# Kernel tuning notes

Hardware: AMD Instinct MI355X
Metric: run time of the kernel (lower is better)

Reference implementation:

```python
import jax, jax.numpy as jnp
import numpy as np

KH, KW = 2, 3          # kernel_size of the masked (shifted) conv
CW = KW // 2           # width padding for order 'A'
B, C, H, W = 8, 32, 256, 256
HID = 64


def _wn(v, g):
    # weight normalization: w = g * v / ||v||, norm over (in, kh, kw) per out channel
    norm = jnp.sqrt(jnp.sum(v * v, axis=(1, 2, 3), keepdims=True))
    return v * (g[:, None, None, None] / norm)


def _conv(x, w, b):
    y = jax.lax.conv_general_dilated(
        x, w, window_strides=(1, 1), padding='VALID',
        dimension_numbers=('NCHW', 'OIHW', 'NCHW'))
    return y + b[None, :, None, None]


def setup_inputs() -> dict:
    key = jax.random.key(0)
    ks = jax.random.split(key, 4)
    x = jax.random.normal(ks[0], (B, C, H, W), dtype=jnp.float32)
    v1 = jax.random.normal(ks[1], (HID, C, KH, KW), dtype=jnp.float32) * 0.05
    g1 = jnp.ones((HID,), dtype=jnp.float32)
    b1 = jnp.zeros((HID,), dtype=jnp.float32)
    v2 = jax.random.normal(ks[2], (2 * C, HID, 1, 1), dtype=jnp.float32) * 0.05
    g2 = jnp.ones((2 * C,), dtype=jnp.float32)
    b2 = jnp.zeros((2 * C,), dtype=jnp.float32)
    return {"x": x, "v1": v1, "g1": g1, "b1": b1, "v2": v2, "g2": g2, "b2": b2}


def reference(x, v1, g1, b1, v2, g2, b2):
    # ShiftedConv2d, order 'A': pad KH rows on top, CW cols each side, drop last
    # row, then VALID conv -> output at row h only sees input rows h-KH..h-1.
    xs = jnp.pad(x, ((0, 0), (0, 0), (KH, 0), (CW, CW)))[:, :, :-1, :]
    h = _conv(xs, _wn(v1, g1), b1)                 # [B, HID, H, W]
    h = jax.nn.elu(h)
    ms = _conv(h, _wn(v2, g2), b2)                 # [B, 2C, H, W]
    mu, log_scale = jnp.split(ms, 2, axis=1)
    scale = jax.nn.sigmoid(log_scale + 2.0)
    out = x * scale + mu                           # affine flow
    logdet = jnp.sum(jnp.log(scale).reshape(x.shape[0], -1), axis=1)  # [B]
    return out, logdet
```

## Files before the change

kernel.cpp:

```cpp
#include <hip/hip_runtime.h>
#include <hip/hip_bf16.h>
#include <math.h>

#define B_   8
#define C_   32
#define H_   256
#define W_   256
#define HW_  (H_*W_)
#define NPIX (B_*C_*H_*W_)

#define PW    260
#define ROWDW (PW*16)
#define ROWB  (ROWDW*4)

typedef __attribute__((ext_vector_type(8))) short short8;
typedef __attribute__((ext_vector_type(4))) float f32x4;
typedef __attribute__((ext_vector_type(2))) float f32x2;

static __device__ __forceinline__ short f2bf(float f) {
    union { __hip_bfloat16 h; short s; } u; u.h = __float2bfloat16(f); return u.s;
}
static __device__ __forceinline__ int cvtpk(float lo, float hi) {
    int r;
    asm("v_cvt_pk_bf16_f32 %0, %1, %2" : "=v"(r) : "v"(lo), "v"(hi));
    return r;
}

__global__ __launch_bounds__(64) void prep_kernel(
    const float* __restrict__ v1, const float* __restrict__ g1,
    const float* __restrict__ v2, const float* __restrict__ g2,
    short* __restrict__ w1b, short* __restrict__ w2b)
{
    const int t   = threadIdx.x;
    const int bid = blockIdx.x;
    if (bid < 64) {
        const int o = bid;
        float a0 = v1[o*192 + t];
        float a1 = v1[o*192 + t + 64];
        float a2 = v1[o*192 + t + 128];
        float s  = a0*a0 + a1*a1 + a2*a2;
        #pragma unroll
        for (int m = 32; m >= 1; m >>= 1) s += __shfl_xor(s, m, 64);
        const float inv = g1[o] / sqrtf(s);
        const int e0 = t, e1 = t + 64, e2 = t + 128;
        w1b[o*192 + (e0%6)*32 + e0/6] = f2bf(a0*inv);
        w1b[o*192 + (e1%6)*32 + e1/6] = f2bf(a1*inv);
        w1b[o*192 + (e2%6)*32 + e2/6] = f2bf(a2*inv);
    } else {
        const int j = bid - 64;
        float a = v2[j*64 + t];
        float s = a*a;
        #pragma unroll
        for (int m = 32; m >= 1; m >>= 1) s += __shfl_xor(s, m, 64);
        const float inv = g2[j] / sqrtf(s);
        const int mt = t >> 4, r = t & 15;
        const int slot = (mt >> 1)*32 + ((r >> 2) << 3) + ((mt & 1) << 2) + (r & 3);
        w2b[j*64 + slot] = f2bf(a*inv);
    }
}

__global__ __launch_bounds__(256) void flow_kernel(
    const float* __restrict__ x,
    const short* __restrict__ w1b, const short* __restrict__ w2b,
    const float* __restrict__ b1,  const float* __restrict__ b2,
    float* __restrict__ out, float* __restrict__ ldpart)
{
    __shared__ int ldsI[2*ROWDW];

    const int bi0 = blockIdx.x;
    const int bi  = (bi0 & 7) * 256 + (bi0 >> 3);
    const int b   = bi >> 8;
    const int h   = bi & 255;

    const int tid  = threadIdx.x;
    const int l    = tid & 63;
    const int wv   = tid >> 6;
    const int lrow = l & 15;
    const int q    = l >> 4;

    const float* xb = x + (size_t)b * (C_*HW_);
    float* ob       = out + (size_t)b * (C_*HW_);

    {
        const int r   = tid >> 7;
        const int hr  = h - 2 + r;
        const int u   = tid & 127;
        const int w0  = u << 1;
        const int p0  = w0 + 1, p1 = w0 + 2;
        const int sw0 = (p0 >> 2) & 3, sw1 = (p1 >> 2) & 3;
        if (hr >= 0) {
            const float* pr = xb + (size_t)hr * W_ + w0;
            #pragma unroll
            for (int g = 0; g < 4; ++g) {
                f32x2 a[8];
                #pragma unroll
                for (int j = 0; j < 8; ++j)
                    a[j] = *(const f32x2*)(pr + (size_t)(8*g + j) * HW_);
                int4 d0, d1;
                d0.x = cvtpk(a[0][0], a[1][0]); d0.y = cvtpk(a[2][0], a[3][0]);
                d0.z = cvtpk(a[4][0], a[5][0]); d0.w = cvtpk(a[6][0], a[7][0]);
                d1.x = cvtpk(a[0][1], a[1][1]); d1.y = cvtpk(a[2][1], a[3][1]);
                d1.z = cvtpk(a[4][1], a[5][1]); d1.w = cvtpk(a[6][1], a[7][1]);
                *(int4*)&ldsI[r*ROWDW + p0*16 + ((g ^ sw0) << 2)] = d0;
                *(int4*)&ldsI[r*ROWDW + p1*16 + ((g ^ sw1) << 2)] = d1;
            }
        } else {
            const int4 z4 = {0,0,0,0};
            #pragma unroll
            for (int g = 0; g < 4; ++g) {
                *(int4*)&ldsI[r*ROWDW + p0*16 + ((g ^ sw0) << 2)] = z4;
                *(int4*)&ldsI[r*ROWDW + p1*16 + ((g ^ sw1) << 2)] = z4;
            }
        }
        if (tid < 16) {
            const int rz = tid >> 3;
            const int pz = ((tid >> 2) & 1) ? 257 : 0;
            *(int4*)&ldsI[rz*ROWDW + pz*16 + ((tid & 3) << 2)] = (int4){0,0,0,0};
        }
    }
    __syncthreads();

    const int cb0 = h*W_ + wv*64 + lrow;
    float xv[8][4];
    #pragma unroll
    for (int jj = 0; jj < 8; ++jj) {
        const int j = (jj >> 2)*16 + 4*q + (jj & 3);
        const float* pxj = xb + (size_t)j * HW_ + cb0;
        #pragma unroll
        for (int nt = 0; nt < 4; ++nt)
            xv[jj][nt] = pxj[nt*16];
    }

    f32x4 acc1[4][4];
    #pragma unroll
    for (int mt = 0; mt < 4; ++mt) {
        const f32x4 bv = *(const f32x4*)(b1 + mt*16 + 4*q);
        #pragma unroll
        for (int nt = 0; nt < 4; ++nt) acc1[mt][nt] = bv;
    }

    #pragma unroll
    for (int tap = 0; tap < 6; ++tap) {
        const int rb = (tap < 3) ? 0 : ROWB;
        const int dw = (tap % 3) - 1;
        short8 wf[4];
        #pragma unroll
        for (int mt = 0; mt < 4; ++mt)
            wf[mt] = *(const short8*)(w1b + (mt*16 + lrow)*192 + tap*32 + q*8);
        #pragma unroll
        for (int nt = 0; nt < 4; ++nt) {
            const int p = wv*64 + nt*16 + lrow + dw + 1;
            const int byteoff = rb + p*64 + ((q ^ ((p >> 2) & 3)) << 4);
            const short8 xf = *(const short8*)((const char*)ldsI + byteoff);
            #pragma unroll
            for (int mt = 0; mt < 4; ++mt)
                acc1[mt][nt] = __builtin_amdgcn_mfma_f32_16x16x32_bf16(
                                   wf[mt], xf, acc1[mt][nt], 0, 0, 0);
        }
    }

    int4 up0[4], up1[4];
    #pragma unroll
    for (int nt = 0; nt < 4; ++nt) {
        float e[16];
        #pragma unroll
        for (int mt = 0; mt < 4; ++mt)
            #pragma unroll
            for (int rg = 0; rg < 4; ++rg) {
                const float v = acc1[mt][nt][rg];
                e[mt*4 + rg] = v > 0.f ? v : (__expf(v) - 1.f);
            }
        up0[nt].x = cvtpk(e[0],  e[1]);  up0[nt].y = cvtpk(e[2],  e[3]);
        up0[nt].z = cvtpk(e[4],  e[5]);  up0[nt].w = cvtpk(e[6],  e[7]);
        up1[nt].x = cvtpk(e[8],  e[9]);  up1[nt].y = cvtpk(e[10], e[11]);
        up1[nt].z = cvtpk(e[12], e[13]); up1[nt].w = cvtpk(e[14], e[15]);
    }

    short8 a2f[2][4];
    #pragma unroll
    for (int kt = 0; kt < 2; ++kt)
        #pragma unroll
        for (int mt2 = 0; mt2 < 4; ++mt2)
            a2f[kt][mt2] = *(const short8*)(w2b + (mt2*16 + lrow)*64 + kt*32 + q*8);

    f32x4 b2m[2], b2s[2];
    #pragma unroll
    for (int mt2 = 0; mt2 < 2; ++mt2) {
        b2m[mt2] = *(const f32x4*)(b2 + mt2*16 + 4*q);
        b2s[mt2] = *(const f32x4*)(b2 + 32 + mt2*16 + 4*q);
    }

    float ldsum = 0.f;
    #pragma unroll
    for (int nt = 0; nt < 4; ++nt) {
        union { int4 i; short8 s; } u0, u1;
        u0.i = up0[nt];
        u1.i = up1[nt];

        f32x4 acc2[4];
        #pragma unroll
        for (int mt2 = 0; mt2 < 4; ++mt2) {
            f32x4 t0 = __builtin_amdgcn_mfma_f32_16x16x32_bf16(
                           a2f[0][mt2], u0.s, (f32x4){0.f,0.f,0.f,0.f}, 0, 0, 0);
            acc2[mt2] = __builtin_amdgcn_mfma_f32_16x16x32_bf16(
                           a2f[1][mt2], u1.s, t0, 0, 0, 0);
        }

        float pr8 = 1.f;
        #pragma unroll
        for (int mt2 = 0; mt2 < 2; ++mt2)
            #pragma unroll
            for (int rg = 0; rg < 4; ++rg) {
                const int jj = mt2*4 + rg;
                const int j  = mt2*16 + 4*q + rg;
                const float mu = acc2[mt2][rg]     + b2m[mt2][rg];
                const float z  = acc2[mt2 + 2][rg] + b2s[mt2][rg] + 2.f;
                const float sc = 1.f / (1.f + __expf(-z));
                pr8 *= sc;
                ob[(size_t)j * HW_ + cb0 + nt*16] = xv[jj][nt] * sc + mu;
            }
        ldsum += __logf(pr8);
    }

    #pragma unroll
    for (int m = 32; m >= 1; m >>= 1) ldsum += __shfl_xor(ldsum, m, 64);
    if (l == 0) ldpart[(size_t)bi * 4 + wv] = ldsum;
}

__global__ __launch_bounds__(256) void reduce_kernel(
    const float* __restrict__ ldpart, float* __restrict__ logdet)
{
    __shared__ float r4[4];
    const int b = blockIdx.x;
    const int t = threadIdx.x;
    const f32x4 v = *(const f32x4*)(ldpart + (size_t)b*1024 + t*4);
    float s = v[0] + v[1] + v[2] + v[3];
    #pragma unroll
    for (int m = 32; m >= 1; m >>= 1) s += __shfl_xor(s, m, 64);
    if ((t & 63) == 0) r4[t >> 6] = s;
    __syncthreads();
    if (t == 0) logdet[b] = r4[0] + r4[1] + r4[2] + r4[3];
}

extern "C" void kernel_launch(void* const* d_in, const int* in_sizes, int n_in,
                              void* d_out, int out_size, void* d_ws, size_t ws_size,
                              hipStream_t stream)
{
    const float* x  = (const float*)d_in[0];
    const float* v1 = (const float*)d_in[1];
    const float* g1 = (const float*)d_in[2];
    const float* b1 = (const float*)d_in[3];
    const float* v2 = (const float*)d_in[4];
    const float* g2 = (const float*)d_in[5];
    const float* b2 = (const float*)d_in[6];

    float* out    = (float*)d_out;
    float* logdet = out + NPIX;

    short* w1b    = (short*)d_ws;
    short* w2b    = w1b + 12288;
    float* ldpart = (float*)((char*)d_ws + 32768);

    prep_kernel<<<128, 64, 0, stream>>>(v1, g1, v2, g2, w1b, w2b);
    flow_kernel<<<B_ * H_, 256, 0, stream>>>(x, w1b, w2b, b1, b2, out, ldpart);
    reduce_kernel<<<B_, 256, 0, stream>>>(ldpart, logdet);
}
```

Measured before the change: 63.04 us.

## Process two output rows per block reusing staged input row in LDS

Each block now computes two consecutive output rows and keeps the shared middle input row resident in a two-slot LDS ring buffer. For the second row it stages only one new row, so each block loads three input rows for two outputs instead of four. The grid is halved and the logdet partial layout and reduce kernel are resized to match. The price is an extra pair of barriers that serialize staging and compute within a block, plus fewer blocks to hide latency.

```diff
diff --git a/kernel.cpp b/kernel.cpp
--- a/kernel.cpp
+++ b/kernel.cpp
@@ -67,10 +67,10 @@
 {
     __shared__ int ldsI[2*ROWDW];
 
-    const int bi0 = blockIdx.x;
-    const int bi  = (bi0 & 7) * 256 + (bi0 >> 3);
-    const int b   = bi >> 8;
-    const int h   = bi & 255;
+    const int bi0  = blockIdx.x;
+    const int b    = bi0 & 7;
+    const int rest = bi0 >> 3;
+    const int h0   = rest << 1;
 
     const int tid  = threadIdx.x;
     const int l    = tid & 63;
@@ -81,17 +81,17 @@
     const float* xb = x + (size_t)b * (C_*HW_);
     float* ob       = out + (size_t)b * (C_*HW_);
 
-    {
-        const int r   = tid >> 7;
-        const int hr  = h - 2 + r;
+    auto stage_row = [&](int hr, int slotdw) {
         const int u   = tid & 127;
         const int w0  = u << 1;
         const int p0  = w0 + 1, p1 = w0 + 2;
         const int sw0 = (p0 >> 2) & 3, sw1 = (p1 >> 2) & 3;
+        const int gb  = (tid >> 7) << 1;
         if (hr >= 0) {
             const float* pr = xb + (size_t)hr * W_ + w0;
             #pragma unroll
-            for (int g = 0; g < 4; ++g) {
+            for (int gg = 0; gg < 2; ++gg) {
+                const int g = gb + gg;
                 f32x2 a[8];
                 #pragma unroll
                 for (int j = 0; j < 8; ++j)
@@ -101,130 +101,146 @@
                 d0.z = cvtpk(a[4][0], a[5][0]); d0.w = cvtpk(a[6][0], a[7][0]);
                 d1.x = cvtpk(a[0][1], a[1][1]); d1.y = cvtpk(a[2][1], a[3][1]);
                 d1.z = cvtpk(a[4][1], a[5][1]); d1.w = cvtpk(a[6][1], a[7][1]);
-                *(int4*)&ldsI[r*ROWDW + p0*16 + ((g ^ sw0) << 2)] = d0;
-                *(int4*)&ldsI[r*ROWDW + p1*16 + ((g ^ sw1) << 2)] = d1;
+                *(int4*)&ldsI[slotdw + p0*16 + ((g ^ sw0) << 2)] = d0;
+                *(int4*)&ldsI[slotdw + p1*16 + ((g ^ sw1) << 2)] = d1;
             }
         } else {
             const int4 z4 = {0,0,0,0};
             #pragma unroll
-            for (int g = 0; g < 4; ++g) {
-                *(int4*)&ldsI[r*ROWDW + p0*16 + ((g ^ sw0) << 2)] = z4;
-                *(int4*)&ldsI[r*ROWDW + p1*16 + ((g ^ sw1) << 2)] = z4;
-            }
-        }
-        if (tid < 16) {
-            const int rz = tid >> 3;
-            const int pz = ((tid >> 2) & 1) ? 257 : 0;
-            *(int4*)&ldsI[rz*ROWDW + pz*16 + ((tid & 3) << 2)] = (int4){0,0,0,0};
-        }
+            for (int gg = 0; gg < 2; ++gg) {
+                const int g = gb + gg;
+                *(int4*)&ldsI[slotdw + p0*16 + ((g ^ sw0) << 2)] = z4;
+                *(int4*)&ldsI[slotdw + p1*16 + ((g ^ sw1) << 2)] = z4;
+            }
+        }
+    };
+
+    auto compute_row = [&](int h, int rbA, int rbB) -> float {
+        const int cb0 = h*W_ + wv*64 + lrow;
+        float xv[8][4];
+        #pragma unroll
+        for (int jj = 0; jj < 8; ++jj) {
+            const int j = (jj >> 2)*16 + 4*q + (jj & 3);
+            const float* pxj = xb + (size_t)j * HW_ + cb0;
+            #pragma unroll
+            for (int nt = 0; nt < 4; ++nt)
+                xv[jj][nt] = pxj[nt*16];
+        }
+
+        f32x4 acc1[4][4];
+        #pragma unroll
+        for (int mt = 0; mt < 4; ++mt) {
+            const f32x4 bv = *(const f32x4*)(b1 + mt*16 + 4*q);
+            #pragma unroll
+            for (int nt = 0; nt < 4; ++nt) acc1[mt][nt] = bv;
+        }
+
+        #pragma unroll
+        for (int tap = 0; tap < 6; ++tap) {
+            const int rb = (tap < 3) ? rbA : rbB;
+            const int dw = (tap % 3) - 1;
+            short8 wf[4];
+            #pragma unroll
+            for (int mt = 0; mt < 4; ++mt)
+                wf[mt] = *(const short8*)(w1b + (mt*16 + lrow)*192 + tap*32 + q*8);
+            #pragma unroll
+            for (int nt = 0; nt < 4; ++nt) {
+                const int p = wv*64 + nt*16 + lrow + dw + 1;
+                const int byteoff = rb + p*64 + ((q ^ ((p >> 2) & 3)) << 4);
+                const short8 xf = *(const short8*)((const char*)ldsI + byteoff);
+                #pragma unroll
+                for (int mt = 0; mt < 4; ++mt)
+                    acc1[mt][nt] = __builtin_amdgcn_mfma_f32_16x16x32_bf16(
+                                       wf[mt], xf, acc1[mt][nt], 0, 0, 0);
+            }
+        }
+
+        int4 up0[4], up1[4];
+        #pragma unroll
+        for (int nt = 0; nt < 4; ++nt) {
+            float e[16];
+            #pragma unroll
+            for (int mt = 0; mt < 4; ++mt)
+                #pragma unroll
+                for (int rg = 0; rg < 4; ++rg) {
+                    const float v = acc1[mt][nt][rg];
+                    e[mt*4 + rg] = v > 0.f ? v : (__expf(v) - 1.f);
+                }
+            up0[nt].x = cvtpk(e[0],  e[1]);  up0[nt].y = cvtpk(e[2],  e[3]);
+            up0[nt].z = cvtpk(e[4],  e[5]);  up0[nt].w = cvtpk(e[6],  e[7]);
+            up1[nt].x = cvtpk(e[8],  e[9]);  up1[nt].y = cvtpk(e[10], e[11]);
+            up1[nt].z = cvtpk(e[12], e[13]); up1[nt].w = cvtpk(e[14], e[15]);
+        }
+
+        short8 a2f[2][4];
+        #pragma unroll
+        for (int kt = 0; kt < 2; ++kt)
+            #pragma unroll
+            for (int mt2 = 0; mt2 < 4; ++mt2)
+                a2f[kt][mt2] = *(const short8*)(w2b + (mt2*16 + lrow)*64 + kt*32 + q*8);
+
+        f32x4 b2m[2], b2s[2];
+        #pragma unroll
+        for (int mt2 = 0; mt2 < 2; ++mt2) {
+            b2m[mt2] = *(const f32x4*)(b2 + mt2*16 + 4*q);
+            b2s[mt2] = *(const f32x4*)(b2 + 32 + mt2*16 + 4*q);
+        }
+
+        float ldsum = 0.f;
+        #pragma unroll
+        for (int nt = 0; nt < 4; ++nt) {
+            union { int4 i; short8 s; } u0, u1;
+            u0.i = up0[nt];
+            u1.i = up1[nt];
+
+            f32x4 acc2[4];
+            #pragma unroll
+            for (int mt2 = 0; mt2 < 4; ++mt2) {
+                f32x4 t0 = __builtin_amdgcn_mfma_f32_16x16x32_bf16(
+                               a2f[0][mt2], u0.s, (f32x4){0.f,0.f,0.f,0.f}, 0, 0, 0);
+                acc2[mt2] = __builtin_amdgcn_mfma_f32_16x16x32_bf16(
+                               a2f[1][mt2], u1.s, t0, 0, 0, 0);
+            }
+
+            float pr8 = 1.f;
+            #pragma unroll
+            for (int mt2 = 0; mt2 < 2; ++mt2)
+                #pragma unroll
+                for (int rg = 0; rg < 4; ++rg) {
+                    const int jj = mt2*4 + rg;
+                    const int j  = mt2*16 + 4*q + rg;
+                    const float mu = acc2[mt2][rg]     + b2m[mt2][rg];
+                    const float z  = acc2[mt2 + 2][rg] + b2s[mt2][rg] + 2.f;
+                    const float sc = 1.f / (1.f + __expf(-z));
+                    pr8 *= sc;
+                    ob[(size_t)j * HW_ + cb0 + nt*16] = xv[jj][nt] * sc + mu;
+                }
+            ldsum += __logf(pr8);
+        }
+        return ldsum;
+    };
+
+    if (tid < 16) {
+        const int sz = tid >> 3;
+        const int pz = ((tid >> 2) & 1) ? 257 : 0;
+        *(int4*)&ldsI[sz*ROWDW + pz*16 + ((tid & 3) << 2)] = (int4){0,0,0,0};
     }
-    __syncthreads();
-
-    const int cb0 = h*W_ + wv*64 + lrow;
-    float xv[8][4];
-    #pragma unroll
-    for (int jj = 0; jj < 8; ++jj) {
-        const int j = (jj >> 2)*16 + 4*q + (jj & 3);
-        const float* pxj = xb + (size_t)j * HW_ + cb0;
-        #pragma unroll
-        for (int nt = 0; nt < 4; ++nt)
-            xv[jj][nt] = pxj[nt*16];
-    }
-
-    f32x4 acc1[4][4];
-    #pragma unroll
-    for (int mt = 0; mt < 4; ++mt) {
-        const f32x4 bv = *(const f32x4*)(b1 + mt*16 + 4*q);
-        #pragma unroll
-        for (int nt = 0; nt < 4; ++nt) acc1[mt][nt] = bv;
-    }
-
-    #pragma unroll
-    for (int tap = 0; tap < 6; ++tap) {
-        const int rb = (tap < 3) ? 0 : ROWB;
-        const int dw = (tap % 3) - 1;
-        short8 wf[4];
-        #pragma unroll
-        for (int mt = 0; mt < 4; ++mt)
-            wf[mt] = *(const short8*)(w1b + (mt*16 + lrow)*192 + tap*32 + q*8);
-        #pragma unroll
-        for (int nt = 0; nt < 4; ++nt) {
-            const int p = wv*64 + nt*16 + lrow + dw + 1;
-            const int byteoff = rb + p*64 + ((q ^ ((p >> 2) & 3)) << 4);
-            const short8 xf = *(const short8*)((const char*)ldsI + byteoff);
-            #pragma unroll
-            for (int mt = 0; mt < 4; ++mt)
-                acc1[mt][nt] = __builtin_amdgcn_mfma_f32_16x16x32_bf16(
-                                   wf[mt], xf, acc1[mt][nt], 0, 0, 0);
-        }
-    }
-
-    int4 up0[4], up1[4];
-    #pragma unroll
-    for (int nt = 0; nt < 4; ++nt) {
-        float e[16];
-        #pragma unroll
-        for (int mt = 0; mt < 4; ++mt)
-            #pragma unroll
-            for (int rg = 0; rg < 4; ++rg) {
-                const float v = acc1[mt][nt][rg];
-                e[mt*4 + rg] = v > 0.f ? v : (__expf(v) - 1.f);
-            }
-        up0[nt].x = cvtpk(e[0],  e[1]);  up0[nt].y = cvtpk(e[2],  e[3]);
-        up0[nt].z = cvtpk(e[4],  e[5]);  up0[nt].w = cvtpk(e[6],  e[7]);
-        up1[nt].x = cvtpk(e[8],  e[9]);  up1[nt].y = cvtpk(e[10], e[11]);
-        up1[nt].z = cvtpk(e[12], e[13]); up1[nt].w = cvtpk(e[14], e[15]);
-    }
-
-    short8 a2f[2][4];
-    #pragma unroll
-    for (int kt = 0; kt < 2; ++kt)
-        #pragma unroll
-        for (int mt2 = 0; mt2 < 4; ++mt2)
-            a2f[kt][mt2] = *(const short8*)(w2b + (mt2*16 + lrow)*64 + kt*32 + q*8);
-
-    f32x4 b2m[2], b2s[2];
-    #pragma unroll
-    for (int mt2 = 0; mt2 < 2; ++mt2) {
-        b2m[mt2] = *(const f32x4*)(b2 + mt2*16 + 4*q);
-        b2s[mt2] = *(const f32x4*)(b2 + 32 + mt2*16 + 4*q);
-    }
-
-    float ldsum = 0.f;
-    #pragma unroll
-    for (int nt = 0; nt < 4; ++nt) {
-        union { int4 i; short8 s; } u0, u1;
-        u0.i = up0[nt];
-        u1.i = up1[nt];
-
-        f32x4 acc2[4];
-        #pragma unroll
-        for (int mt2 = 0; mt2 < 4; ++mt2) {
-            f32x4 t0 = __builtin_amdgcn_mfma_f32_16x16x32_bf16(
-                           a2f[0][mt2], u0.s, (f32x4){0.f,0.f,0.f,0.f}, 0, 0, 0);
-            acc2[mt2] = __builtin_amdgcn_mfma_f32_16x16x32_bf16(
-                           a2f[1][mt2], u1.s, t0, 0, 0, 0);
-        }
-
-        float pr8 = 1.f;
-        #pragma unroll
-        for (int mt2 = 0; mt2 < 2; ++mt2)
-            #pragma unroll
-            for (int rg = 0; rg < 4; ++rg) {
-                const int jj = mt2*4 + rg;
-                const int j  = mt2*16 + 4*q + rg;
-                const float mu = acc2[mt2][rg]     + b2m[mt2][rg];
-                const float z  = acc2[mt2 + 2][rg] + b2s[mt2][rg] + 2.f;
-                const float sc = 1.f / (1.f + __expf(-z));
-                pr8 *= sc;
-                ob[(size_t)j * HW_ + cb0 + nt*16] = xv[jj][nt] * sc + mu;
-            }
-        ldsum += __logf(pr8);
-    }
+
+    stage_row(h0 - 2, 0);
+    stage_row(h0 - 1, ROWDW);
+    __syncthreads();
+
+    float ldsum = compute_row(h0, 0, ROWB);
+    __syncthreads();
+
+    stage_row(h0, 0);
+    __syncthreads();
+
+    ldsum += compute_row(h0 + 1, ROWB, 0);
 
     #pragma unroll
     for (int m = 32; m >= 1; m >>= 1) ldsum += __shfl_xor(ldsum, m, 64);
-    if (l == 0) ldpart[(size_t)bi * 4 + wv] = ldsum;
+    if (l == 0) ldpart[(size_t)b * 512 + rest * 4 + wv] = ldsum;
 }
 
 __global__ __launch_bounds__(256) void reduce_kernel(
@@ -233,8 +249,8 @@
     __shared__ float r4[4];
     const int b = blockIdx.x;
     const int t = threadIdx.x;
-    const f32x4 v = *(const f32x4*)(ldpart + (size_t)b*1024 + t*4);
-    float s = v[0] + v[1] + v[2] + v[3];
+    const f32x2 v = *(const f32x2*)(ldpart + (size_t)b*512 + t*2);
+    float s = v[0] + v[1];
     #pragma unroll
     for (int m = 32; m >= 1; m >>= 1) s += __shfl_xor(s, m, 64);
     if ((t & 63) == 0) r4[t >> 6] = s;
@@ -262,6 +278,6 @@
     float* ldpart = (float*)((char*)d_ws + 32768);
 
     prep_kernel<<<128, 64, 0, stream>>>(v1, g1, v2, g2, w1b, w2b);
-    flow_kernel<<<B_ * H_, 256, 0, stream>>>(x, w1b, w2b, b1, b2, out, ldpart);
+    flow_kernel<<<B_ * (H_/2), 256, 0, stream>>>(x, w1b, w2b, b1, b2, out, ldpart);
     reduce_kernel<<<B_, 256, 0, stream>>>(ldpart, logdet);
 }
```

Result: slower. 83.17 us (+31.9%).

## Retile flow blocks to two output rows by half width with three-row LDS halo

Applied to the files above, without the earlier changes.

Each block now computes two consecutive output rows over a 128-pixel half width instead of one full row. It stages three input rows (plus explicit left/right halo columns loaded from global) into LDS, so the two rows share the middle input row. This lowers redundant global reads and bf16 conversion of input rows per output row, from 2x to 1.5x. The cost is extra halo-column logic and a different block-to-(batch,row) mapping that affects L2 locality.

```diff
diff --git a/kernel.cpp b/kernel.cpp
--- a/kernel.cpp
+++ b/kernel.cpp
@@ -9,9 +9,9 @@
 #define HW_  (H_*W_)
 #define NPIX (B_*C_*H_*W_)
 
-#define PW    260
-#define ROWDW (PW*16)
-#define ROWB  (ROWDW*4)
+#define SLOTS5  130
+#define SLOTDW  (SLOTS5*16)
+#define SLOTB   (SLOTDW*4)
 
 typedef __attribute__((ext_vector_type(8))) short short8;
 typedef __attribute__((ext_vector_type(4))) float f32x4;
@@ -65,12 +65,13 @@
     const float* __restrict__ b1,  const float* __restrict__ b2,
     float* __restrict__ out, float* __restrict__ ldpart)
 {
-    __shared__ int ldsI[2*ROWDW];
-
-    const int bi0 = blockIdx.x;
-    const int bi  = (bi0 & 7) * 256 + (bi0 >> 3);
-    const int b   = bi >> 8;
-    const int h   = bi & 255;
+    __shared__ int ldsI[3*SLOTDW];
+
+    const int bi0  = blockIdx.x;
+    const int b    = bi0 & 7;
+    const int rest = bi0 >> 3;
+    const int h0   = (rest >> 1) << 1;
+    const int pxb  = (rest & 1) << 7;
 
     const int tid  = threadIdx.x;
     const int l    = tid & 63;
@@ -81,15 +82,15 @@
     const float* xb = x + (size_t)b * (C_*HW_);
     float* ob       = out + (size_t)b * (C_*HW_);
 
-    {
-        const int r   = tid >> 7;
-        const int hr  = h - 2 + r;
-        const int u   = tid & 127;
-        const int w0  = u << 1;
-        const int p0  = w0 + 1, p1 = w0 + 2;
+    if (tid < 192) {
+        const int r   = tid >> 6;
+        const int hr  = h0 - 2 + r;
+        const int u   = tid & 63;
+        const int p0  = 2*u + 1, p1 = 2*u + 2;
         const int sw0 = (p0 >> 2) & 3, sw1 = (p1 >> 2) & 3;
+        const int sb  = r * SLOTDW;
         if (hr >= 0) {
-            const float* pr = xb + (size_t)hr * W_ + w0;
+            const float* pr = xb + (size_t)hr * W_ + (pxb + 2*u);
             #pragma unroll
             for (int g = 0; g < 4; ++g) {
                 f32x2 a[8];
@@ -101,26 +102,49 @@
                 d0.z = cvtpk(a[4][0], a[5][0]); d0.w = cvtpk(a[6][0], a[7][0]);
                 d1.x = cvtpk(a[0][1], a[1][1]); d1.y = cvtpk(a[2][1], a[3][1]);
                 d1.z = cvtpk(a[4][1], a[5][1]); d1.w = cvtpk(a[6][1], a[7][1]);
-                *(int4*)&ldsI[r*ROWDW + p0*16 + ((g ^ sw0) << 2)] = d0;
-                *(int4*)&ldsI[r*ROWDW + p1*16 + ((g ^ sw1) << 2)] = d1;
+                *(int4*)&ldsI[sb + p0*16 + ((g ^ sw0) << 2)] = d0;
+                *(int4*)&ldsI[sb + p1*16 + ((g ^ sw1) << 2)] = d1;
             }
         } else {
             const int4 z4 = {0,0,0,0};
             #pragma unroll
             for (int g = 0; g < 4; ++g) {
-                *(int4*)&ldsI[r*ROWDW + p0*16 + ((g ^ sw0) << 2)] = z4;
-                *(int4*)&ldsI[r*ROWDW + p1*16 + ((g ^ sw1) << 2)] = z4;
-            }
-        }
-        if (tid < 16) {
-            const int rz = tid >> 3;
-            const int pz = ((tid >> 2) & 1) ? 257 : 0;
-            *(int4*)&ldsI[rz*ROWDW + pz*16 + ((tid & 3) << 2)] = (int4){0,0,0,0};
+                *(int4*)&ldsI[sb + p0*16 + ((g ^ sw0) << 2)] = z4;
+                *(int4*)&ldsI[sb + p1*16 + ((g ^ sw1) << 2)] = z4;
+            }
+        }
+    } else {
+        const int e0 = tid - 192;
+        #pragma unroll
+        for (int k = 0; k < 2; ++k) {
+            const int e = e0 + (k << 6);
+            if (e < 96) {
+                const int rz  = e >> 5;
+                const int rem = e & 31;
+                const int hc  = rem >> 4;
+                const int c2  = rem & 15;
+                const int wc  = hc ? (pxb + 128) : (pxb - 1);
+                const int pz  = hc ? 129 : 0;
+                const int hz  = h0 - 2 + rz;
+                int d = 0;
+                if (hz >= 0 && wc >= 0 && wc < W_) {
+                    const float a0 = xb[(size_t)(2*c2  )*HW_ + (size_t)hz*W_ + wc];
+                    const float a1 = xb[(size_t)(2*c2+1)*HW_ + (size_t)hz*W_ + wc];
+                    d = cvtpk(a0, a1);
+                }
+                ldsI[rz*SLOTDW + pz*16 + c2] = d;
+            }
         }
     }
     __syncthreads();
 
-    const int cb0 = h*W_ + wv*64 + lrow;
+    const int rsel = wv >> 1;
+    const int h    = h0 + rsel;
+    const int pxl  = (wv & 1) << 6;
+    const int rbA  = rsel * SLOTB;
+    const int rbB  = (rsel + 1) * SLOTB;
+
+    const int cb0 = h*W_ + pxb + pxl + lrow;
     float xv[8][4];
     #pragma unroll
     for (int jj = 0; jj < 8; ++jj) {
@@ -141,7 +165,7 @@
 
     #pragma unroll
     for (int tap = 0; tap < 6; ++tap) {
-        const int rb = (tap < 3) ? 0 : ROWB;
+        const int rb = (tap < 3) ? rbA : rbB;
         const int dw = (tap % 3) - 1;
         short8 wf[4];
         #pragma unroll
@@ -149,7 +173,7 @@
             wf[mt] = *(const short8*)(w1b + (mt*16 + lrow)*192 + tap*32 + q*8);
         #pragma unroll
         for (int nt = 0; nt < 4; ++nt) {
-            const int p = wv*64 + nt*16 + lrow + dw + 1;
+            const int p = pxl + nt*16 + lrow + dw + 1;
             const int byteoff = rb + p*64 + ((q ^ ((p >> 2) & 3)) << 4);
             const short8 xf = *(const short8*)((const char*)ldsI + byteoff);
             #pragma unroll
@@ -224,7 +248,7 @@
 
     #pragma unroll
     for (int m = 32; m >= 1; m >>= 1) ldsum += __shfl_xor(ldsum, m, 64);
-    if (l == 0) ldpart[(size_t)bi * 4 + wv] = ldsum;
+    if (l == 0) ldpart[(size_t)b * 1024 + rest * 4 + wv] = ldsum;
 }
 
 __global__ __launch_bounds__(256) void reduce_kernel(
@@ -262,6 +286,6 @@
     float* ldpart = (float*)((char*)d_ws + 32768);
 
     prep_kernel<<<128, 64, 0, stream>>>(v1, g1, v2, g2, w1b, w2b);
-    flow_kernel<<<B_ * H_, 256, 0, stream>>>(x, w1b, w2b, b1, b2, out, ldpart);
+    flow_kernel<<<B_ * (H_/2) * 2, 256, 0, stream>>>(x, w1b, w2b, b1, b2, out, ldpart);
     reduce_kernel<<<B_, 256, 0, stream>>>(ldpart, logdet);
 }
```

Measured after the change: 63.83 us. Within noise of the previous version (+1.2%).
